# Performance work log

Measured on AMD Instinct MI355X. Metric: run time of the kernel, lower is better.

## Reference

```python
import jax, jax.numpy as jnp
import numpy as np

B, N, FEAT, H, E, L = 4096, 64, 32, 128, 4, 3  # batch, node_num, node feat, hidden_dim, edge_dim, hidden_num


def setup_inputs() -> dict:
    key = jax.random.key(0)
    ks = jax.random.split(key, 12)
    s = 0.05
    x = jax.random.normal(ks[0], (B, N, FEAT), dtype=jnp.float32)
    adj = jax.random.uniform(ks[1], (B, E, N, N), dtype=jnp.float32)
    # per-node input/output embeddings (stacked over node index)
    in_w = jax.random.normal(ks[2], (N, FEAT, H), dtype=jnp.float32) * s
    in_b = jax.random.normal(ks[3], (N, H), dtype=jnp.float32) * s
    out_w = jax.random.normal(ks[4], (N, H, FEAT), dtype=jnp.float32) * s
    out_b = jax.random.normal(ks[5], (N, FEAT), dtype=jnp.float32) * s
    # relational GC weights per layer: (L, E, H, H) and bias (L, E, 1, H)
    gc_w = jax.random.normal(ks[6], (L, E, H, H), dtype=jnp.float32) * s
    gc_b = jax.random.normal(ks[7], (L, E, 1, H), dtype=jnp.float32) * s
    # GRU params, gate order [r, z, n] like torch
    w_ih = jax.random.normal(ks[8], (3 * H, H), dtype=jnp.float32) * s
    w_hh = jax.random.normal(ks[9], (3 * H, H), dtype=jnp.float32) * s
    b_ih = jax.random.normal(ks[10], (3 * H,), dtype=jnp.float32) * s
    b_hh = jax.random.normal(ks[11], (3 * H,), dtype=jnp.float32) * s
    return {"x": x, "adj": adj, "in_w": in_w, "in_b": in_b, "out_w": out_w,
            "out_b": out_b, "gc_w": gc_w, "gc_b": gc_b, "w_ih": w_ih,
            "w_hh": w_hh, "b_ih": b_ih, "b_hh": b_hh}


def _gru_step(xf, h, w_ih, w_hh, b_ih, b_hh):
    # xf, h: (B*N, H); single-timestep torch GRU cell
    gi = xf @ w_ih.T + b_ih
    gh = h @ w_hh.T + b_hh
    i_r, i_z, i_n = jnp.split(gi, 3, axis=-1)
    h_r, h_z, h_n = jnp.split(gh, 3, axis=-1)
    r = jax.nn.sigmoid(i_r + h_r)
    z = jax.nn.sigmoid(i_z + h_z)
    n = jnp.tanh(i_n + r * h_n)
    return (1.0 - z) * n + z * h


def reference(x, adj, in_w, in_b, out_w, out_b, gc_w, gc_b, w_ih, w_hh, b_ih, b_hh):
    # per-node input embedding: (B, N, FEAT) -> (B, N, H)
    h = jnp.einsum('bnd,ndh->bnh', x, in_w) + in_b
    hidden = h.reshape(-1, H)  # initial GRU hidden = embedded input
    cur = h
    for i in range(L):
        # relational GCN: per-edge-type projection + adjacency matmul + bias + relu + mean over edge types
        support = jnp.einsum('bid,edh->beih', cur, gc_w[i])
        out = jnp.einsum('beij,bejh->beih', adj, support) + gc_b[i]
        out = jax.nn.relu(out)
        agg = jnp.mean(out, axis=1)  # (B, N, H)
        hidden = _gru_step(agg.reshape(-1, H), hidden, w_ih, w_hh, b_ih, b_hh)
        cur = hidden.reshape(B, N, H)
    # per-node output embedding, zero-padded back to hidden width
    feats = jnp.einsum('bnh,nhd->bnd', cur, out_w) + out_b  # (B, N, FEAT)
    return jnp.pad(feats, ((0, 0), (0, 0), (0, H - FEAT)))
```

## Files before the change

kernel.cpp:

```cpp
#include <hip/hip_runtime.h>
#include <cstdint>

#define NBATCH 4096
#define NNODE  64
#define FEAT   32
#define H      128
#define NE     4
#define NL     3

typedef __attribute__((ext_vector_type(8))) short short8;
typedef __attribute__((ext_vector_type(4))) short short4v;
typedef __attribute__((ext_vector_type(4))) float f32x4;
typedef __attribute__((ext_vector_type(2))) float f32x2;

#define IMG_GC_ELEMS   (128 * 64)
#define IMG_GRU_ELEMS  (48 * 128)
#define IMG_GC_BYTES   (24 * IMG_GC_ELEMS * 2)
#define IMG_GRU_BYTES  (16 * IMG_GRU_ELEMS * 2)
#define WS_NEEDED      (IMG_GC_BYTES + IMG_GRU_BYTES)

__device__ __forceinline__ unsigned short f2b(float f) {
  union { float f; unsigned u; } v; v.f = f;
  unsigned u = v.u + 0x7FFFu + ((v.u >> 16) & 1u);
  return (unsigned short)(u >> 16);
}
__device__ __forceinline__ float b2f(unsigned short s) {
  union { unsigned u; float f; } v; v.u = ((unsigned)s) << 16;
  return v.f;
}
__device__ __forceinline__ float sigm(float v) { return 1.0f / (1.0f + __expf(-v)); }
__device__ __forceinline__ float tanh_(float v) {
  v = fminf(fmaxf(v, -15.f), 15.f);
  float e = __expf(-2.f * v);
  return (1.f - e) / (1.f + e);
}
__device__ __forceinline__ int gidx128(int r, int g) { return r * 128 + ((g ^ (r & 7)) << 3); }
__device__ __forceinline__ int idx128(int r, int k) { return gidx128(r, k >> 3) + (k & 7); }
__device__ __forceinline__ int gidx64(int r, int g) { return r * 64 + (((g ^ (r & 7)) & 7) << 3); }

__device__ __forceinline__ short8 pack8(const float* v) {
  short8 r;
  #pragma unroll
  for (int j = 0; j < 8; ++j) r[j] = (short)f2b(v[j]);
  return r;
}

__device__ __forceinline__ void gll16(const void* g, void* l) {
  __builtin_amdgcn_global_load_lds(
      (const __attribute__((address_space(1))) unsigned int*)g,
      (__attribute__((address_space(3))) unsigned int*)l, 16, 0, 0);
}

#define STAGE(dst, src, NIT)                                             \
  do {                                                                   \
    _Pragma("unroll")                                                    \
    for (int it_ = 0; it_ < (NIT); ++it_) {                              \
      int off_ = (it_ * 4 + w) * 1024;                                   \
      gll16((const char*)(src) + off_ + lane * 16, (char*)(dst) + off_); \
    }                                                                    \
  } while (0)

__global__ __launch_bounds__(256, 2) void k_prep(
    const float* __restrict__ gc_w, const float* __restrict__ w_ih,
    const float* __restrict__ w_hh, unsigned short* __restrict__ ws)
{
  const int t = threadIdx.x;
  if (blockIdx.x < 24) {
    const int blk = blockIdx.x;
    const int kh = blk & 1, e = (blk >> 1) & 3, l = blk >> 3;
    const float* We = gc_w + (size_t)(l * NE + e) * H * H;
    unsigned short* dst = ws + (size_t)blk * IMG_GC_ELEMS;
    #pragma unroll
    for (int it = 0; it < 4; ++it) {
      int idx = t + it * 256;
      int r = idx >> 3, g = idx & 7;
      float v[8];
      #pragma unroll
      for (int j = 0; j < 8; ++j) v[j] = We[(kh * 64 + g * 8 + j) * H + r];
      *(short8*)&dst[gidx64(r, g)] = pack8(v);
    }
  } else {
    const int blk = blockIdx.x - 24;
    const int c = blk & 7, m = blk >> 3;
    const float* Mat = m ? w_hh : w_ih;
    unsigned short* dst = ws + IMG_GC_BYTES / 2 + (size_t)blk * IMG_GRU_ELEMS;
    #pragma unroll
    for (int it = 0; it < 3; ++it) {
      int idx = t + it * 256;
      int rr = idx >> 4, g = idx & 15;
      int mrow = (rr >> 4) * H + 16 * c + (rr & 15);
      float v[8];
      #pragma unroll
      for (int j = 0; j < 8; ++j) v[j] = Mat[mrow * H + g * 8 + j];
      *(short8*)&dst[gidx128(rr, g)] = pack8(v);
    }
  }
}

__global__ __launch_bounds__(256, 2) void k_inemb(
    const float* __restrict__ x, const float* __restrict__ in_w,
    const float* __restrict__ in_b, float* __restrict__ out)
{
  __shared__ float s_wt[FEAT * H];
  __shared__ float s_x[64 * FEAT];
  const int t = threadIdx.x;
  const int n = blockIdx.x >> 6, bt = blockIdx.x & 63, b0 = bt * 64;
  const float* wsrc = in_w + (size_t)n * FEAT * H;
  #pragma unroll
  for (int it = 0; it < 4; ++it) {
    int i4 = t + it * 256;
    *(f32x4*)&s_wt[i4 * 4] = *(const f32x4*)&wsrc[i4 * 4];
  }
  {
    int r = t >> 2, q = t & 3;
    const float* xs = x + ((size_t)(b0 + r) * NNODE + n) * FEAT;
    *(f32x4*)&s_x[r * 32 + q * 8]     = *(const f32x4*)&xs[q * 8];
    *(f32x4*)&s_x[r * 32 + q * 8 + 4] = *(const f32x4*)&xs[q * 8 + 4];
  }
  __syncthreads();
  const int h2 = t & 63, rp = t >> 6;
  const float bi0 = in_b[n * H + 2 * h2], bi1 = in_b[n * H + 2 * h2 + 1];
  #pragma unroll 1
  for (int m = 0; m < 16; ++m) {
    int r = rp + 4 * m;
    float a0 = bi0, a1 = bi1;
    #pragma unroll
    for (int d = 0; d < 32; ++d) {
      float xv = s_x[r * 32 + d];
      f32x2 wv = *(const f32x2*)&s_wt[d * H + 2 * h2];
      a0 += xv * wv.x; a1 += xv * wv.y;
    }
    unsigned p = (unsigned)f2b(a0) | ((unsigned)f2b(a1) << 16);
    unsigned short* tail = (unsigned short*)(out + ((size_t)(b0 + r) * NNODE + n) * H + 64);
    *(unsigned*)(tail + 2 * h2) = p;
  }
}

__global__ __launch_bounds__(256, 2) void k_main(
    const float* __restrict__ adj,
    const float* __restrict__ gc_b,
    const float* __restrict__ b_ih, const float* __restrict__ b_hh,
    const unsigned short* __restrict__ wimg,
    float* __restrict__ out)
{
  __shared__ unsigned short s_cur[64 * 128];
  __shared__ unsigned short s_u[128 * 64];
  __shared__ unsigned short s_w0[128 * 64];
  __shared__ unsigned short s_w1[128 * 64];
  __shared__ unsigned short s_adj[64 * 64];
  __shared__ float s_bias[1280];

  const int t = threadIdx.x;
  const int b = blockIdx.x;
  const int w = t >> 6, lane = t & 63, lr = lane & 15, lq = lane >> 4;
  float* outb = out + (size_t)b * NNODE * H;
  const unsigned short* img_gru = wimg + IMG_GC_BYTES / 2;

  STAGE(s_w0, wimg, 4);
  #pragma unroll
  for (int it = 0; it < 4; ++it) {
    int idx = t + it * 256;
    int n = idx >> 4, g = idx & 15;
    short8 v = *(const short8*)((const unsigned short*)(outb + n * H + 64) + g * 8);
    *(short8*)&s_cur[gidx128(n, g)] = v;
  }
  #pragma unroll
  for (int it = 0; it < 3; ++it) {
    int idx = t + it * 256;
    s_bias[512 + idx] = (idx < 384) ? b_ih[idx] : b_hh[idx - 384];
  }
  __syncthreads();

  #pragma unroll 1
  for (int layer = 0; layer < NL; ++layer) {
    f32x4 agg[8];
    #pragma unroll
    for (int tn = 0; tn < 8; ++tn) agg[tn] = f32x4{0.f, 0.f, 0.f, 0.f};

    #pragma unroll 1
    for (int e = 0; e < NE; ++e) {
      const unsigned short* img_e = wimg + (size_t)((layer * NE + e) * 2) * IMG_GC_ELEMS;
      const float* adj_e = adj + (((size_t)b * NE + e) * NNODE * NNODE);

      STAGE(s_w1, img_e + IMG_GC_ELEMS, 4);
      if (e == 0) {
        s_bias[t]       = gc_b[layer * 512 + t];
        s_bias[t + 256] = gc_b[layer * 512 + t + 256];
      }
      #pragma unroll
      for (int it = 0; it < 2; ++it) {
        int idx = t + it * 256;
        int i = idx >> 3, g = idx & 7;
        const float* src = adj_e + i * 64 + g * 8;
        float v[8];
        #pragma unroll
        for (int j = 0; j < 8; ++j) v[j] = src[j];
        *(short8*)&s_adj[gidx64(i, g)] = pack8(v);
      }
      f32x4 Sacc[8];
      #pragma unroll
      for (int tn = 0; tn < 8; ++tn) Sacc[tn] = f32x4{0.f, 0.f, 0.f, 0.f};
      #pragma unroll
      for (int ks = 0; ks < 2; ++ks) {
        short8 a = *(const short8*)&s_cur[gidx128(16 * w + lr, ks * 4 + lq)];
        #pragma unroll
        for (int tn = 0; tn < 8; ++tn) {
          short8 bb = *(const short8*)&s_w0[gidx64(16 * tn + lr, ks * 4 + lq)];
          Sacc[tn] = __builtin_amdgcn_mfma_f32_16x16x32_bf16(a, bb, Sacc[tn], 0, 0, 0);
        }
      }
      __syncthreads();

      if (e < 3) { STAGE(s_w0, img_e + 2 * IMG_GC_ELEMS, 4); }
      else       { STAGE(s_w0, img_gru, 3); }
      #pragma unroll
      for (int ks = 0; ks < 2; ++ks) {
        short8 a = *(const short8*)&s_cur[gidx128(16 * w + lr, 8 + ks * 4 + lq)];
        #pragma unroll
        for (int tn = 0; tn < 8; ++tn) {
          short8 bb = *(const short8*)&s_w1[gidx64(16 * tn + lr, ks * 4 + lq)];
          Sacc[tn] = __builtin_amdgcn_mfma_f32_16x16x32_bf16(a, bb, Sacc[tn], 0, 0, 0);
        }
      }
      {
        int nb = 16 * w + 4 * lq;
        int g = nb >> 3, sub = nb & 7;
        #pragma unroll
        for (int tn = 0; tn < 8; ++tn) {
          int h = 16 * tn + lr;
          short4v p;
          #pragma unroll
          for (int r = 0; r < 4; ++r) p[r] = (short)f2b(Sacc[tn][r]);
          *(short4v*)&s_u[gidx64(h, g) + sub] = p;
        }
      }
      __syncthreads();

      {
        f32x4 Oacc[8];
        #pragma unroll
        for (int tn = 0; tn < 8; ++tn) Oacc[tn] = f32x4{0.f, 0.f, 0.f, 0.f};
        #pragma unroll
        for (int ks = 0; ks < 2; ++ks) {
          short8 a = *(const short8*)&s_adj[gidx64(16 * w + lr, ks * 4 + lq)];
          #pragma unroll
          for (int tn = 0; tn < 8; ++tn) {
            short8 bb = *(const short8*)&s_u[gidx64(16 * tn + lr, ks * 4 + lq)];
            Oacc[tn] = __builtin_amdgcn_mfma_f32_16x16x32_bf16(a, bb, Oacc[tn], 0, 0, 0);
          }
        }
        #pragma unroll
        for (int tn = 0; tn < 8; ++tn) {
          float bias = s_bias[e * 128 + 16 * tn + lr];
          #pragma unroll
          for (int r = 0; r < 4; ++r)
            agg[tn][r] += 0.25f * fmaxf(Oacc[tn][r] + bias, 0.f);
        }
      }
      __syncthreads();
    }

    #pragma unroll
    for (int tn = 0; tn < 8; ++tn) {
      int h = 16 * tn + lr;
      #pragma unroll
      for (int r = 0; r < 4; ++r) {
        int i = 16 * w + 4 * lq + r;
        s_u[idx128(i, h)] = f2b(agg[tn][r]);
      }
    }
    __syncthreads();

    #pragma unroll 1
    for (int c = 0; c < 8; ++c) {
      STAGE(s_w1, img_gru + (size_t)(8 + c) * IMG_GRU_ELEMS, 3);
      f32x4 gi[3], gh[3];
      #pragma unroll
      for (int tg = 0; tg < 3; ++tg) gi[tg] = f32x4{0.f, 0.f, 0.f, 0.f};
      #pragma unroll
      for (int ks = 0; ks < 4; ++ks) {
        short8 bb = *(const short8*)&s_u[gidx128(16 * w + lr, ks * 4 + lq)];
        #pragma unroll
        for (int tg = 0; tg < 3; ++tg) {
          short8 a = *(const short8*)&s_w0[gidx128(16 * tg + lr, ks * 4 + lq)];
          gi[tg] = __builtin_amdgcn_mfma_f32_16x16x32_bf16(a, bb, gi[tg], 0, 0, 0);
        }
      }
      __syncthreads();

      if (c < 7)          { STAGE(s_w0, img_gru + (size_t)(c + 1) * IMG_GRU_ELEMS, 3); }
      else if (layer < 2) { STAGE(s_w0, wimg + (size_t)((layer + 1) * NE * 2) * IMG_GC_ELEMS, 4); }
      #pragma unroll
      for (int tg = 0; tg < 3; ++tg) gh[tg] = f32x4{0.f, 0.f, 0.f, 0.f};
      #pragma unroll
      for (int ks = 0; ks < 4; ++ks) {
        short8 bb = *(const short8*)&s_cur[gidx128(16 * w + lr, ks * 4 + lq)];
        #pragma unroll
        for (int tg = 0; tg < 3; ++tg) {
          short8 a = *(const short8*)&s_w1[gidx128(16 * tg + lr, ks * 4 + lq)];
          gh[tg] = __builtin_amdgcn_mfma_f32_16x16x32_bf16(a, bb, gh[tg], 0, 0, 0);
        }
      }
      {
        int i = 16 * w + lr;
        int g = (16 * c + 4 * lq) >> 3;
        int off = gidx128(i, g) + ((4 * lq) & 7);
        short4v hv = *(const short4v*)&s_cur[off];
        short4v hp;
        #pragma unroll
        for (int r = 0; r < 4; ++r) {
          int mH = 16 * c + 4 * lq + r;
          float rg = sigm(gi[0][r] + s_bias[512 + mH] + gh[0][r] + s_bias[896 + mH]);
          float zg = sigm(gi[1][r] + s_bias[640 + mH] + gh[1][r] + s_bias[1024 + mH]);
          float ng = tanh_(gi[2][r] + s_bias[768 + mH] + rg * (gh[2][r] + s_bias[1152 + mH]));
          float hold = b2f((unsigned short)hv[r]);
          hp[r] = (short)f2b((1.f - zg) * ng + zg * hold);
        }
        unsigned short* tail = (unsigned short*)(outb + (size_t)i * H + 64);
        *(short4v*)(tail + 16 * c + 4 * lq) = hp;
      }
      __syncthreads();
    }

    if (layer < 2) {
      #pragma unroll
      for (int it = 0; it < 4; ++it) {
        int idx = t + it * 256;
        int n = idx >> 4, g = idx & 15;
        short8 v = *(const short8*)((const unsigned short*)(outb + n * H + 64) + g * 8);
        *(short8*)&s_cur[gidx128(n, g)] = v;
      }
      __syncthreads();
    }
  }
}

__global__ __launch_bounds__(256, 2) void k_outemb(
    const float* __restrict__ out_w, const float* __restrict__ out_b,
    float* __restrict__ out)
{
  __shared__ float s_wt[H * FEAT];
  __shared__ float s_c[64 * 132];
  const int t = threadIdx.x;
  const int n = blockIdx.x >> 6, bt = blockIdx.x & 63, b0 = bt * 64;
  const float* wsrc = out_w + (size_t)n * H * FEAT;
  #pragma unroll
  for (int it = 0; it < 4; ++it) {
    int i4 = t + it * 256;
    *(f32x4*)&s_wt[i4 * 4] = *(const f32x4*)&wsrc[i4 * 4];
  }
  #pragma unroll
  for (int it = 0; it < 4; ++it) {
    int idx = t + it * 256;
    int r = idx >> 4, g = idx & 15;
    const unsigned short* tail =
        (const unsigned short*)(out + ((size_t)(b0 + r) * NNODE + n) * H + 64);
    short8 v = *(const short8*)(tail + g * 8);
    #pragma unroll
    for (int j = 0; j < 8; ++j) s_c[r * 132 + g * 8 + j] = b2f((unsigned short)v[j]);
  }
  __syncthreads();
  const int d = t & 31, rq = t >> 5;
  const float bias = out_b[n * FEAT + d];
  float accs[8];
  #pragma unroll
  for (int m = 0; m < 8; ++m) {
    int r = rq + 8 * m;
    float a = bias;
    #pragma unroll 8
    for (int k = 0; k < H; ++k) a += s_c[r * 132 + k] * s_wt[k * FEAT + d];
    accs[m] = a;
  }
  #pragma unroll
  for (int m = 0; m < 8; ++m) {
    int r = rq + 8 * m;
    out[((size_t)(b0 + r) * NNODE + n) * H + d] = accs[m];
  }
  #pragma unroll
  for (int q = 0; q < 6; ++q) {
    int idx = t + q * 256;
    int r = idx / 24, c4 = idx - r * 24;
    *(f32x4*)&out[((size_t)(b0 + r) * NNODE + n) * H + FEAT + c4 * 4] =
        f32x4{0.f, 0.f, 0.f, 0.f};
  }
}

extern "C" void kernel_launch(void* const* d_in, const int* in_sizes, int n_in,
                              void* d_out, int out_size, void* d_ws, size_t ws_size,
                              hipStream_t stream) {
  const float* x     = (const float*)d_in[0];
  const float* adj   = (const float*)d_in[1];
  const float* in_w  = (const float*)d_in[2];
  const float* in_b  = (const float*)d_in[3];
  const float* out_w = (const float*)d_in[4];
  const float* out_b = (const float*)d_in[5];
  const float* gc_w  = (const float*)d_in[6];
  const float* gc_b  = (const float*)d_in[7];
  const float* w_ih  = (const float*)d_in[8];
  const float* w_hh  = (const float*)d_in[9];
  const float* b_ih  = (const float*)d_in[10];
  const float* b_hh  = (const float*)d_in[11];
  (void)in_sizes; (void)n_in; (void)out_size;
  unsigned short* wimg = (unsigned short*)d_ws;
  hipLaunchKernelGGL(k_inemb, dim3(NBATCH), dim3(256), 0, stream, x, in_w, in_b, (float*)d_out);
  hipLaunchKernelGGL(k_prep, dim3(40), dim3(256), 0, stream, gc_w, w_ih, w_hh, wimg);
  hipLaunchKernelGGL(k_main, dim3(NBATCH), dim3(256), 0, stream,
                     adj, gc_b, b_ih, b_hh, wimg, (float*)d_out);
  hipLaunchKernelGGL(k_outemb, dim3(NBATCH), dim3(256), 0, stream, out_w, out_b, (float*)d_out);
}
```

Measured before the change: 826.7 us.

## Pre-convert adjacency to bf16 image and async-stage it in main kernel

When the workspace is large enough, k_inemb also converts each batch's fp32 adjacency into a swizzled bf16 image in workspace. k_main then loads it asynchronously into LDS with global_load_lds instead of doing synchronous fp32 loads and packing. The barriers are replaced with explicit vmcnt and lgkmcnt waits so the staged loads overlap compute. Other changes are hardware bf16 pack instructions, setprio around MFMA blocks, and 64-bit packed stores. This trades an extra bf16 adjacency write and re-read for less load latency in the main loop, and it depends on the workspace size to take the fast path.

```diff
diff --git a/kernel.cpp b/kernel.cpp
--- a/kernel.cpp
+++ b/kernel.cpp
@@ -12,12 +12,16 @@
 typedef __attribute__((ext_vector_type(4))) short short4v;
 typedef __attribute__((ext_vector_type(4))) float f32x4;
 typedef __attribute__((ext_vector_type(2))) float f32x2;
+typedef unsigned long long u64;
 
 #define IMG_GC_ELEMS   (128 * 64)
 #define IMG_GRU_ELEMS  (48 * 128)
 #define IMG_GC_BYTES   (24 * IMG_GC_ELEMS * 2)
 #define IMG_GRU_BYTES  (16 * IMG_GRU_ELEMS * 2)
-#define WS_NEEDED      (IMG_GC_BYTES + IMG_GRU_BYTES)
+#define WS_W_BYTES     (IMG_GC_BYTES + IMG_GRU_BYTES)
+#define WIMG_SHORTS    (WS_W_BYTES / 2)
+#define ADJ_IMG_ELEMS  4096
+#define WS_FULL ((size_t)WS_W_BYTES + (size_t)NBATCH * NE * ADJ_IMG_ELEMS * 2)
 
 __device__ __forceinline__ unsigned short f2b(float f) {
   union { float f; unsigned u; } v; v.f = f;
@@ -27,6 +31,11 @@
 __device__ __forceinline__ float b2f(unsigned short s) {
   union { unsigned u; float f; } v; v.u = ((unsigned)s) << 16;
   return v.f;
+}
+__device__ __forceinline__ unsigned cvtpk(float lo, float hi) {
+  unsigned r;
+  asm volatile("v_cvt_pk_bf16_f32 %0, %1, %2" : "=v"(r) : "v"(lo), "v"(hi));
+  return r;
 }
 __device__ __forceinline__ float sigm(float v) { return 1.0f / (1.0f + __expf(-v)); }
 __device__ __forceinline__ float tanh_(float v) {
@@ -38,11 +47,11 @@
 __device__ __forceinline__ int idx128(int r, int k) { return gidx128(r, k >> 3) + (k & 7); }
 __device__ __forceinline__ int gidx64(int r, int g) { return r * 64 + (((g ^ (r & 7)) & 7) << 3); }
 
-__device__ __forceinline__ short8 pack8(const float* v) {
-  short8 r;
-  #pragma unroll
-  for (int j = 0; j < 8; ++j) r[j] = (short)f2b(v[j]);
-  return r;
+__device__ __forceinline__ short8 pack8f(const float* v) {
+  union { unsigned u[4]; short8 s; } r;
+  r.u[0] = cvtpk(v[0], v[1]); r.u[1] = cvtpk(v[2], v[3]);
+  r.u[2] = cvtpk(v[4], v[5]); r.u[3] = cvtpk(v[6], v[7]);
+  return r.s;
 }
 
 __device__ __forceinline__ void gll16(const void* g, void* l) {
@@ -59,6 +68,12 @@
       gll16((const char*)(src) + off_ + lane * 16, (char*)(dst) + off_); \
     }                                                                    \
   } while (0)
+
+#define BAR() do { asm volatile("s_waitcnt lgkmcnt(0)" ::: "memory"); \
+                   __builtin_amdgcn_s_barrier(); } while (0)
+#define VMW(N) do { asm volatile("s_waitcnt vmcnt(" #N ")" ::: "memory"); \
+                    __builtin_amdgcn_sched_barrier(0); } while (0)
+#define SB0() __builtin_amdgcn_sched_barrier(0)
 
 __global__ __launch_bounds__(256, 2) void k_prep(
     const float* __restrict__ gc_w, const float* __restrict__ w_ih,
@@ -77,13 +92,13 @@
       float v[8];
       #pragma unroll
       for (int j = 0; j < 8; ++j) v[j] = We[(kh * 64 + g * 8 + j) * H + r];
-      *(short8*)&dst[gidx64(r, g)] = pack8(v);
+      *(short8*)&dst[gidx64(r, g)] = pack8f(v);
     }
   } else {
     const int blk = blockIdx.x - 24;
     const int c = blk & 7, m = blk >> 3;
     const float* Mat = m ? w_hh : w_ih;
-    unsigned short* dst = ws + IMG_GC_BYTES / 2 + (size_t)blk * IMG_GRU_ELEMS;
+    unsigned short* dst = ws + WIMG_SHORTS - IMG_GRU_BYTES / 2 + (size_t)blk * IMG_GRU_ELEMS;
     #pragma unroll
     for (int it = 0; it < 3; ++it) {
       int idx = t + it * 256;
@@ -92,14 +107,16 @@
       float v[8];
       #pragma unroll
       for (int j = 0; j < 8; ++j) v[j] = Mat[mrow * H + g * 8 + j];
-      *(short8*)&dst[gidx128(rr, g)] = pack8(v);
-    }
-  }
-}
-
+      *(short8*)&dst[gidx128(rr, g)] = pack8f(v);
+    }
+  }
+}
+
+template <bool ADJIMG>
 __global__ __launch_bounds__(256, 2) void k_inemb(
     const float* __restrict__ x, const float* __restrict__ in_w,
-    const float* __restrict__ in_b, float* __restrict__ out)
+    const float* __restrict__ in_b, const float* __restrict__ adj,
+    unsigned short* __restrict__ ws, float* __restrict__ out)
 {
   __shared__ float s_wt[FEAT * H];
   __shared__ float s_x[64 * FEAT];
@@ -130,12 +147,27 @@
       f32x2 wv = *(const f32x2*)&s_wt[d * H + 2 * h2];
       a0 += xv * wv.x; a1 += xv * wv.y;
     }
-    unsigned p = (unsigned)f2b(a0) | ((unsigned)f2b(a1) << 16);
+    unsigned p = cvtpk(a0, a1);
     unsigned short* tail = (unsigned short*)(out + ((size_t)(b0 + r) * NNODE + n) * H + 64);
     *(unsigned*)(tail + 2 * h2) = p;
   }
-}
-
+  if (ADJIMG) {
+    const float* ab = adj + (size_t)blockIdx.x * NE * NNODE * NNODE;
+    unsigned short* dst = ws + WIMG_SHORTS + (size_t)blockIdx.x * NE * ADJ_IMG_ELEMS;
+    #pragma unroll 1
+    for (int q = 0; q < 8; ++q) {
+      int gi = t + q * 256;
+      int e = gi >> 9, idx = gi & 511, r = idx >> 3, g = idx & 7;
+      const float* src = ab + e * 4096 + r * 64 + g * 8;
+      float v[8];
+      #pragma unroll
+      for (int j = 0; j < 8; ++j) v[j] = src[j];
+      *(short8*)&dst[e * ADJ_IMG_ELEMS + gidx64(r, g)] = pack8f(v);
+    }
+  }
+}
+
+template <bool ADJIMG>
 __global__ __launch_bounds__(256, 2) void k_main(
     const float* __restrict__ adj,
     const float* __restrict__ gc_b,
@@ -154,7 +186,8 @@
   const int b = blockIdx.x;
   const int w = t >> 6, lane = t & 63, lr = lane & 15, lq = lane >> 4;
   float* outb = out + (size_t)b * NNODE * H;
-  const unsigned short* img_gru = wimg + IMG_GC_BYTES / 2;
+  const unsigned short* img_gru = wimg + WIMG_SHORTS - IMG_GRU_BYTES / 2;
+  const unsigned short* aimg = wimg + WIMG_SHORTS + (size_t)b * NE * ADJ_IMG_ELEMS;
 
   STAGE(s_w0, wimg, 4);
   #pragma unroll
@@ -180,26 +213,33 @@
     #pragma unroll 1
     for (int e = 0; e < NE; ++e) {
       const unsigned short* img_e = wimg + (size_t)((layer * NE + e) * 2) * IMG_GC_ELEMS;
-      const float* adj_e = adj + (((size_t)b * NE + e) * NNODE * NNODE);
-
-      STAGE(s_w1, img_e + IMG_GC_ELEMS, 4);
+
       if (e == 0) {
         s_bias[t]       = gc_b[layer * 512 + t];
         s_bias[t + 256] = gc_b[layer * 512 + t + 256];
       }
-      #pragma unroll
-      for (int it = 0; it < 2; ++it) {
-        int idx = t + it * 256;
-        int i = idx >> 3, g = idx & 7;
-        const float* src = adj_e + i * 64 + g * 8;
-        float v[8];
-        #pragma unroll
-        for (int j = 0; j < 8; ++j) v[j] = src[j];
-        *(short8*)&s_adj[gidx64(i, g)] = pack8(v);
+      STAGE(s_w1, img_e + IMG_GC_ELEMS, 4);
+      SB0();
+      if (ADJIMG) {
+        STAGE(s_adj, aimg + (size_t)e * ADJ_IMG_ELEMS, 2);
+        SB0();
+      } else {
+        const float* adj_e = adj + (((size_t)b * NE + e) * NNODE * NNODE);
+        #pragma unroll
+        for (int it = 0; it < 2; ++it) {
+          int idx = t + it * 256;
+          int i = idx >> 3, g = idx & 7;
+          const float* src = adj_e + i * 64 + g * 8;
+          float v[8];
+          #pragma unroll
+          for (int j = 0; j < 8; ++j) v[j] = src[j];
+          *(short8*)&s_adj[gidx64(i, g)] = pack8f(v);
+        }
       }
       f32x4 Sacc[8];
       #pragma unroll
       for (int tn = 0; tn < 8; ++tn) Sacc[tn] = f32x4{0.f, 0.f, 0.f, 0.f};
+      __builtin_amdgcn_s_setprio(1);
       #pragma unroll
       for (int ks = 0; ks < 2; ++ks) {
         short8 a = *(const short8*)&s_cur[gidx128(16 * w + lr, ks * 4 + lq)];
@@ -209,10 +249,15 @@
           Sacc[tn] = __builtin_amdgcn_mfma_f32_16x16x32_bf16(a, bb, Sacc[tn], 0, 0, 0);
         }
       }
-      __syncthreads();
+      __builtin_amdgcn_s_setprio(0);
+      if (ADJIMG) { VMW(2); }
+      else        { VMW(0); }
+      BAR();
 
       if (e < 3) { STAGE(s_w0, img_e + 2 * IMG_GC_ELEMS, 4); }
       else       { STAGE(s_w0, img_gru, 3); }
+      SB0();
+      __builtin_amdgcn_s_setprio(1);
       #pragma unroll
       for (int ks = 0; ks < 2; ++ks) {
         short8 a = *(const short8*)&s_cur[gidx128(16 * w + lr, 8 + ks * 4 + lq)];
@@ -222,24 +267,26 @@
           Sacc[tn] = __builtin_amdgcn_mfma_f32_16x16x32_bf16(a, bb, Sacc[tn], 0, 0, 0);
         }
       }
+      __builtin_amdgcn_s_setprio(0);
       {
         int nb = 16 * w + 4 * lq;
         int g = nb >> 3, sub = nb & 7;
         #pragma unroll
         for (int tn = 0; tn < 8; ++tn) {
           int h = 16 * tn + lr;
-          short4v p;
-          #pragma unroll
-          for (int r = 0; r < 4; ++r) p[r] = (short)f2b(Sacc[tn][r]);
-          *(short4v*)&s_u[gidx64(h, g) + sub] = p;
-        }
-      }
-      __syncthreads();
+          u64 pv = (u64)cvtpk(Sacc[tn][0], Sacc[tn][1]) |
+                   ((u64)cvtpk(Sacc[tn][2], Sacc[tn][3]) << 32);
+          *(u64*)&s_u[gidx64(h, g) + sub] = pv;
+        }
+      }
+      VMW(4);
+      BAR();
 
       {
         f32x4 Oacc[8];
         #pragma unroll
         for (int tn = 0; tn < 8; ++tn) Oacc[tn] = f32x4{0.f, 0.f, 0.f, 0.f};
+        __builtin_amdgcn_s_setprio(1);
         #pragma unroll
         for (int ks = 0; ks < 2; ++ks) {
           short8 a = *(const short8*)&s_adj[gidx64(16 * w + lr, ks * 4 + lq)];
@@ -249,6 +296,7 @@
             Oacc[tn] = __builtin_amdgcn_mfma_f32_16x16x32_bf16(a, bb, Oacc[tn], 0, 0, 0);
           }
         }
+        __builtin_amdgcn_s_setprio(0);
         #pragma unroll
         for (int tn = 0; tn < 8; ++tn) {
           float bias = s_bias[e * 128 + 16 * tn + lr];
@@ -257,7 +305,8 @@
             agg[tn][r] += 0.25f * fmaxf(Oacc[tn][r] + bias, 0.f);
         }
       }
-      __syncthreads();
+      VMW(0);
+      BAR();
     }
 
     #pragma unroll
@@ -269,7 +318,7 @@
         s_u[idx128(i, h)] = f2b(agg[tn][r]);
       }
     }
-    __syncthreads();
+    BAR();
 
     #pragma unroll 1
     for (int c = 0; c < 8; ++c) {
@@ -277,6 +326,7 @@
       f32x4 gi[3], gh[3];
       #pragma unroll
       for (int tg = 0; tg < 3; ++tg) gi[tg] = f32x4{0.f, 0.f, 0.f, 0.f};
+      __builtin_amdgcn_s_setprio(1);
       #pragma unroll
       for (int ks = 0; ks < 4; ++ks) {
         short8 bb = *(const short8*)&s_u[gidx128(16 * w + lr, ks * 4 + lq)];
@@ -286,12 +336,14 @@
           gi[tg] = __builtin_amdgcn_mfma_f32_16x16x32_bf16(a, bb, gi[tg], 0, 0, 0);
         }
       }
+      __builtin_amdgcn_s_setprio(0);
       __syncthreads();
 
       if (c < 7)          { STAGE(s_w0, img_gru + (size_t)(c + 1) * IMG_GRU_ELEMS, 3); }
       else if (layer < 2) { STAGE(s_w0, wimg + (size_t)((layer + 1) * NE * 2) * IMG_GC_ELEMS, 4); }
       #pragma unroll
       for (int tg = 0; tg < 3; ++tg) gh[tg] = f32x4{0.f, 0.f, 0.f, 0.f};
+      __builtin_amdgcn_s_setprio(1);
       #pragma unroll
       for (int ks = 0; ks < 4; ++ks) {
         short8 bb = *(const short8*)&s_cur[gidx128(16 * w + lr, ks * 4 + lq)];
@@ -301,12 +353,13 @@
           gh[tg] = __builtin_amdgcn_mfma_f32_16x16x32_bf16(a, bb, gh[tg], 0, 0, 0);
         }
       }
+      __builtin_amdgcn_s_setprio(0);
       {
         int i = 16 * w + lr;
         int g = (16 * c + 4 * lq) >> 3;
         int off = gidx128(i, g) + ((4 * lq) & 7);
         short4v hv = *(const short4v*)&s_cur[off];
-        short4v hp;
+        float hf[4];
         #pragma unroll
         for (int r = 0; r < 4; ++r) {
           int mH = 16 * c + 4 * lq + r;
@@ -314,10 +367,11 @@
           float zg = sigm(gi[1][r] + s_bias[640 + mH] + gh[1][r] + s_bias[1024 + mH]);
           float ng = tanh_(gi[2][r] + s_bias[768 + mH] + rg * (gh[2][r] + s_bias[1152 + mH]));
           float hold = b2f((unsigned short)hv[r]);
-          hp[r] = (short)f2b((1.f - zg) * ng + zg * hold);
-        }
+          hf[r] = (1.f - zg) * ng + zg * hold;
+        }
+        u64 hp = (u64)cvtpk(hf[0], hf[1]) | ((u64)cvtpk(hf[2], hf[3]) << 32);
         unsigned short* tail = (unsigned short*)(outb + (size_t)i * H + 64);
-        *(short4v*)(tail + 16 * c + 4 * lq) = hp;
+        *(u64*)(tail + 16 * c + 4 * lq) = hp;
       }
       __syncthreads();
     }
@@ -402,9 +456,18 @@
   const float* b_hh  = (const float*)d_in[11];
   (void)in_sizes; (void)n_in; (void)out_size;
   unsigned short* wimg = (unsigned short*)d_ws;
-  hipLaunchKernelGGL(k_inemb, dim3(NBATCH), dim3(256), 0, stream, x, in_w, in_b, (float*)d_out);
+  const bool full = ws_size >= WS_FULL;
   hipLaunchKernelGGL(k_prep, dim3(40), dim3(256), 0, stream, gc_w, w_ih, w_hh, wimg);
-  hipLaunchKernelGGL(k_main, dim3(NBATCH), dim3(256), 0, stream,
-                     adj, gc_b, b_ih, b_hh, wimg, (float*)d_out);
+  if (full) {
+    hipLaunchKernelGGL(k_inemb<true>, dim3(NBATCH), dim3(256), 0, stream,
+                       x, in_w, in_b, adj, wimg, (float*)d_out);
+    hipLaunchKernelGGL(k_main<true>, dim3(NBATCH), dim3(256), 0, stream,
+                       adj, gc_b, b_ih, b_hh, wimg, (float*)d_out);
+  } else {
+    hipLaunchKernelGGL(k_inemb<false>, dim3(NBATCH), dim3(256), 0, stream,
+                       x, in_w, in_b, adj, wimg, (float*)d_out);
+    hipLaunchKernelGGL(k_main<false>, dim3(NBATCH), dim3(256), 0, stream,
+                       adj, gc_b, b_ih, b_hh, wimg, (float*)d_out);
+  }
   hipLaunchKernelGGL(k_outemb, dim3(NBATCH), dim3(256), 0, stream, out_w, out_b, (float*)d_out);
 }
```

Measured after the change: 823.8 us. No clear change (-0.4%).
